# Kernel tuning notes

Hardware: AMD Instinct MI355X
Metric: run time of the kernel (lower is better)

Reference implementation:

```python
import jax, jax.numpy as jnp
import numpy as np

B, C_IN, C_OUT, A, H, W = 32, 256, 512, 256, 64, 64


def setup_inputs() -> dict:
    key = jax.random.key(0)
    ks = jax.random.split(key, 8)
    s = 0.02
    return {
        "x": jax.random.normal(ks[0], (B, C_IN, H, W), dtype=jnp.float32),
        "g": jax.random.normal(ks[1], (B, C_OUT), dtype=jnp.float32),
        "Wg": jax.random.normal(ks[2], (A, C_OUT), dtype=jnp.float32) * s,
        "bg": jnp.full((A,), 0.1, dtype=jnp.float32),
        "Wx": jax.random.normal(ks[3], (A, C_IN), dtype=jnp.float32) * s,
        "bx": jnp.full((A,), 0.1, dtype=jnp.float32),
        "Wf": jax.random.normal(ks[4], (1, A), dtype=jnp.float32) * s,
        "bf": jnp.full((1,), 0.1, dtype=jnp.float32),
    }


def reference(x, g, Wg, bg, Wx, bx, Wf, bf):
    b, c, h, w = x.shape
    gg = g @ Wg.T + bg                                  # [B, A]
    xf = x.reshape(b, c, h * w)                          # [B, C, HW]
    # Linear_x applied per spatial position (batched instead of python loop)
    nx = jnp.einsum('bcn,ac->bna', xf, Wx) + bx          # [B, HW, A]
    nx = jax.nn.relu(gg[:, None, :] + nx)                # [B, HW, A]
    att = jnp.einsum('bna,a->bn', nx, Wf[0]) + bf[0]     # [B, HW]
    # min-subtract, sum-divide normalization
    att = att - jnp.min(att, axis=1, keepdims=True)
    att = att / jnp.sum(att, axis=1, keepdims=True)
    out = jnp.einsum('bcn,bn->bc', xf, att)              # weighted pooling [B, C]
    return out, att.reshape(b, h, w)
```

## Files before the change

### kernel.cpp

```cpp
#include <hip/hip_runtime.h>
#include <stdint.h>

#define B_   32
#define CIN  256
#define COUT 512
#define A_   256
#define HW_  4096
#define NT   64

typedef short  short8  __attribute__((ext_vector_type(8)));
typedef float  float4_ __attribute__((ext_vector_type(4)));

__device__ __forceinline__ unsigned f2bf(float f) {
    unsigned u = __float_as_uint(f);
    u += 0x7FFFu + ((u >> 16) & 1u);
    return u >> 16;
}
__device__ __forceinline__ float bf2f(unsigned h) {
    return __uint_as_float(h << 16);
}

__global__ __launch_bounds__(256) void prep_kernel(
    const float* __restrict__ g, const float* __restrict__ Wg,
    const float* __restrict__ bg, const float* __restrict__ Wx,
    const float* __restrict__ bx,
    uint4* __restrict__ WxR, float* __restrict__ ggbx,
    float* __restrict__ P, float* __restrict__ T)
{
    int t = threadIdx.x;
    if (blockIdx.x >= 32) {
        int e = (blockIdx.x - 32) * 256 + t;
        int lane = e & 63, ai = (e >> 6) & 3, kk = (e >> 8) & 7, w = e >> 11;
        int a  = w * 64 + ai * 16 + (lane & 15);
        int kb = kk * 32 + (lane >> 4) * 8;
        const float4* s = (const float4*)(Wx + (size_t)a * 256 + kb);
        float4 u0 = s[0], u1 = s[1];
        uint4 pk;
        pk.x = f2bf(u0.x) | (f2bf(u0.y) << 16);
        pk.y = f2bf(u0.z) | (f2bf(u0.w) << 16);
        pk.z = f2bf(u1.x) | (f2bf(u1.y) << 16);
        pk.w = f2bf(u1.z) | (f2bf(u1.w) << 16);
        WxR[e] = pk;
        return;
    }
    int b = blockIdx.x;
    int i = b * 256 + t;
    P[i] = 0.f; T[i] = 0.f;

    __shared__ float gl[COUT];
    gl[t]       = g[b * COUT + t];
    gl[t + 256] = g[b * COUT + 256 + t];
    __syncthreads();

    float acc0 = bg[t] + bx[t], acc1 = 0.f;
    const float4* wr = (const float4*)(Wg + (size_t)t * COUT);
    #pragma unroll 8
    for (int co = 0; co < COUT / 4; co += 2) {
        float4 wv0 = wr[co],     gv0 = *(const float4*)&gl[co * 4];
        float4 wv1 = wr[co + 1], gv1 = *(const float4*)&gl[co * 4 + 4];
        acc0 += wv0.x * gv0.x + wv0.y * gv0.y + wv0.z * gv0.z + wv0.w * gv0.w;
        acc1 += wv1.x * gv1.x + wv1.y * gv1.y + wv1.z * gv1.z + wv1.w * gv1.w;
    }
    ggbx[b * 256 + t] = acc0 + acc1;
}

__global__ __launch_bounds__(256, 4) void attn_main(
    const float* __restrict__ x, const char* __restrict__ WxR,
    const float* __restrict__ ggbx, const float* __restrict__ Wf,
    const float* __restrict__ bfs,
    float* __restrict__ P, float* __restrict__ T, float* __restrict__ raw)
{
    __shared__ unsigned int xT[NT * 128];
    __shared__ float att_part[4][NT];
    __shared__ float raw_l[NT];

    int bid = blockIdx.x;
    int b = bid >> 6, nt = bid & 63;
    int t = threadIdx.x, w = t >> 6, lane = t & 63;
    int quad = lane >> 4, l15 = lane & 15;

    const float* xb = x + (size_t)b * CIN * HW_ + nt * NT;

    {
        int sub = lane >> 4;
        int n4  = (lane & 15) * 4;
        int cb0 = w * 64 + sub * 8;
        int cb1 = cb0 + 32;
        float4_ v[16];
        #pragma unroll
        for (int j = 0; j < 8; j++)
            v[j] = *(const float4_*)(xb + (size_t)(cb0 + j) * HW_ + n4);
        #pragma unroll
        for (int j = 0; j < 8; j++)
            v[8 + j] = *(const float4_*)(xb + (size_t)(cb1 + j) * HW_ + n4);

        #pragma unroll
        for (int gq = 0; gq < 2; gq++) {
            int q = (gq ? cb1 : cb0) >> 3;
            const float4_* vg = &v[gq * 8];
            #pragma unroll
            for (int r = 0; r < 4; r++) {
                uint4 pk;
                pk.x = f2bf(vg[0][r]) | (f2bf(vg[1][r]) << 16);
                pk.y = f2bf(vg[2][r]) | (f2bf(vg[3][r]) << 16);
                pk.z = f2bf(vg[4][r]) | (f2bf(vg[5][r]) << 16);
                pk.w = f2bf(vg[6][r]) | (f2bf(vg[7][r]) << 16);
                int n = n4 + r;
                *(uint4*)&xT[n * 128 + ((q ^ (n & 31)) << 2)] = pk;
            }
        }
    }

    float ga[4], wfv[4];
    #pragma unroll
    for (int ai = 0; ai < 4; ai++) {
        int a = w * 64 + ai * 16 + l15;
        ga[ai]  = ggbx[b * 256 + a];
        wfv[ai] = Wf[a];
    }
    __syncthreads();

    float4_ acc[4][4];
    #pragma unroll
    for (int mi = 0; mi < 4; mi++)
        #pragma unroll
        for (int ai = 0; ai < 4; ai++)
            acc[mi][ai] = (float4_){0.f, 0.f, 0.f, 0.f};

    const char* wsl = WxR + w * 32768 + lane * 16;
    short8 afA[4], bfA[4], afB[4], bfB[4];

    auto LD = [&](short8* af, short8* bf, int k0) {
        int qk = (k0 >> 3) + quad;
        #pragma unroll
        for (int mi = 0; mi < 4; mi++) {
            int n = mi * 16 + l15;
            af[mi] = *(const short8*)&xT[n * 128 + ((qk ^ (n & 31)) << 2)];
        }
        const char* wk = wsl + (k0 >> 5) * 4096;
        #pragma unroll
        for (int ai = 0; ai < 4; ai++)
            bf[ai] = *(const short8*)(wk + ai * 1024);
    };
    auto MM = [&](short8* af, short8* bf) {
        #pragma unroll
        for (int mi = 0; mi < 4; mi++)
            #pragma unroll
            for (int ai = 0; ai < 4; ai++)
                acc[mi][ai] = __builtin_amdgcn_mfma_f32_16x16x32_bf16(
                    af[mi], bf[ai], acc[mi][ai], 0, 0, 0);
    };

    LD(afA, bfA, 0);   LD(afB, bfB, 32);
    MM(afA, bfA);      LD(afA, bfA, 64);
    MM(afB, bfB);      LD(afB, bfB, 96);
    MM(afA, bfA);      LD(afA, bfA, 128);
    MM(afB, bfB);      LD(afB, bfB, 160);
    MM(afA, bfA);      LD(afA, bfA, 192);
    MM(afB, bfB);      LD(afB, bfB, 224);
    MM(afA, bfA);
    MM(afB, bfB);

    #pragma unroll
    for (int mi = 0; mi < 4; mi++) {
        float p[4] = {0.f, 0.f, 0.f, 0.f};
        #pragma unroll
        for (int ai = 0; ai < 4; ai++) {
            #pragma unroll
            for (int r = 0; r < 4; r++) {
                float vv = acc[mi][ai][r] + ga[ai];
                vv = fmaxf(vv, 0.f);
                p[r] = fmaf(vv, wfv[ai], p[r]);
            }
        }
        #pragma unroll
        for (int r = 0; r < 4; r++) {
            #pragma unroll
            for (int off = 1; off < 16; off <<= 1)
                p[r] += __shfl_xor(p[r], off, 16);
        }
        if (l15 == 0) {
            #pragma unroll
            for (int r = 0; r < 4; r++)
                att_part[w][mi * 16 + quad * 4 + r] = p[r];
        }
    }
    __syncthreads();

    if (t < NT) {
        float rv = att_part[0][t] + att_part[1][t] + att_part[2][t] + att_part[3][t] + bfs[0];
        raw[b * HW_ + nt * NT + t] = rv;
        raw_l[t] = rv;
    }
    __syncthreads();

    float pp[4] = {0.f, 0.f, 0.f, 0.f};
    float tt[4] = {0.f, 0.f, 0.f, 0.f};
    {
        int q    = (t & 63) >> 1;
        int half = (t & 1) * 8;
        int nb   = (t >> 6) * 16;
        #pragma unroll
        for (int i = 0; i < 16; i++) {
            int n = nb + i;
            uint2 u = *(const uint2*)((const char*)xT + n * 512 + ((q ^ (n & 31)) << 4) + half);
            float rv = raw_l[n];
            float x0 = bf2f(u.x & 0xFFFFu), x1 = bf2f(u.x >> 16);
            float x2 = bf2f(u.y & 0xFFFFu), x3 = bf2f(u.y >> 16);
            pp[0] = fmaf(x0, rv, pp[0]); tt[0] += x0;
            pp[1] = fmaf(x1, rv, pp[1]); tt[1] += x1;
            pp[2] = fmaf(x2, rv, pp[2]); tt[2] += x2;
            pp[3] = fmaf(x3, rv, pp[3]); tt[3] += x3;
        }
    }
    __syncthreads();
    {
        float* red = (float*)xT;
        float4_* pr = (float4_*)(red + w * 512);
        float4_* tr = (float4_*)(red + w * 512 + 256);
        pr[t & 63] = (float4_){pp[0], pp[1], pp[2], pp[3]};
        tr[t & 63] = (float4_){tt[0], tt[1], tt[2], tt[3]};
        __syncthreads();
        float Pc = red[t] + red[512 + t] + red[1024 + t] + red[1536 + t];
        float Tc = red[256 + t] + red[768 + t] + red[1280 + t] + red[1792 + t];
        atomicAdd(&P[b * 256 + t], Pc);
        atomicAdd(&T[b * 256 + t], Tc);
    }
}

__global__ __launch_bounds__(256) void finalize_kernel(
    const float* __restrict__ raw, const float* __restrict__ P,
    const float* __restrict__ T, float* __restrict__ out)
{
    int b = blockIdx.x, t = threadIdx.x;
    const float* r = raw + (size_t)b * HW_;
    float v[16];
    float mn = 3.4e38f, sm = 0.f;
    #pragma unroll
    for (int i = 0; i < 16; i++) {
        v[i] = r[t + 256 * i];
        mn = fminf(mn, v[i]);
        sm += v[i];
    }
    #pragma unroll
    for (int off = 1; off < 64; off <<= 1) {
        mn = fminf(mn, __shfl_xor(mn, off, 64));
        sm += __shfl_xor(sm, off, 64);
    }
    __shared__ float smn[4], ssm[4];
    int w = t >> 6;
    if ((t & 63) == 0) { smn[w] = mn; ssm[w] = sm; }
    __syncthreads();
    mn = fminf(fminf(smn[0], smn[1]), fminf(smn[2], smn[3]));
    sm = (ssm[0] + ssm[1]) + (ssm[2] + ssm[3]);
    float S = sm - 4096.f * mn;
    float inv = 1.f / S;

    float* att = out + B_ * CIN + (size_t)b * HW_;
    #pragma unroll
    for (int i = 0; i < 16; i++) att[t + 256 * i] = (v[i] - mn) * inv;

    int ic = b * 256 + t;
    out[ic] = (P[ic] - mn * T[ic]) * inv;
}

extern "C" void kernel_launch(void* const* d_in, const int* in_sizes, int n_in,
                              void* d_out, int out_size, void* d_ws, size_t ws_size,
                              hipStream_t stream)
{
    const float* x   = (const float*)d_in[0];
    const float* g   = (const float*)d_in[1];
    const float* Wg  = (const float*)d_in[2];
    const float* bg  = (const float*)d_in[3];
    const float* Wx  = (const float*)d_in[4];
    const float* bx  = (const float*)d_in[5];
    const float* Wf  = (const float*)d_in[6];
    const float* bf  = (const float*)d_in[7];
    float* out = (float*)d_out;

    char* wsb = (char*)d_ws;
    uint4* WxR  = (uint4*)wsb;
    float* ggbx = (float*)(wsb + 131072);
    float* P    = ggbx + 8192;
    float* T    = P + 8192;
    float* raw  = T + 8192;

    prep_kernel<<<64, 256, 0, stream>>>(g, Wg, bg, Wx, bx, WxR, ggbx, P, T);
    attn_main<<<2048, 256, 0, stream>>>(x, (const char*)WxR, ggbx, Wf, bf, P, T, raw);
    finalize_kernel<<<32, 256, 0, stream>>>(raw, P, T, out);
}
```

Baseline: 242.8 us.

## Stage x tile in LDS as fp32 via direct global-to-LDS loads

Replaces the register-staged fp32-to-bf16 transpose of the x tile with direct global_load_lds copies into a 64KB fp32 LDS tile. The bf16 conversion moves into the MFMA A-fragment loads, which now do scalar strided LDS reads and pack pairs per K step. The weighted-pooling epilogue reads the fp32 tile directly and uses shuffle reductions with per-channel atomics instead of a cross-wave LDS reduction. LDS use doubles, so occupancy is lowered to 2 blocks per CU. The conversion work and LDS reads in the MMA loop grow, and the atomic count rises.

```diff
diff --git a/kernel.cpp b/kernel.cpp
--- a/kernel.cpp
+++ b/kernel.cpp
@@ -4,7 +4,6 @@
 #define B_   32
 #define CIN  256
 #define COUT 512
-#define A_   256
 #define HW_  4096
 #define NT   64
 
@@ -15,9 +14,6 @@
     unsigned u = __float_as_uint(f);
     u += 0x7FFFu + ((u >> 16) & 1u);
     return u >> 16;
-}
-__device__ __forceinline__ float bf2f(unsigned h) {
-    return __uint_as_float(h << 16);
 }
 
 __global__ __launch_bounds__(256) void prep_kernel(
@@ -64,13 +60,13 @@
     ggbx[b * 256 + t] = acc0 + acc1;
 }
 
-__global__ __launch_bounds__(256, 4) void attn_main(
+__global__ __launch_bounds__(256, 2) void attn_main(
     const float* __restrict__ x, const char* __restrict__ WxR,
     const float* __restrict__ ggbx, const float* __restrict__ Wf,
     const float* __restrict__ bfs,
     float* __restrict__ P, float* __restrict__ T, float* __restrict__ raw)
 {
-    __shared__ unsigned int xT[NT * 128];
+    __shared__ float xTf[CIN * NT];
     __shared__ float att_part[4][NT];
     __shared__ float raw_l[NT];
 
@@ -82,32 +78,14 @@
     const float* xb = x + (size_t)b * CIN * HW_ + nt * NT;
 
     {
-        int sub = lane >> 4;
-        int n4  = (lane & 15) * 4;
-        int cb0 = w * 64 + sub * 8;
-        int cb1 = cb0 + 32;
-        float4_ v[16];
-        #pragma unroll
-        for (int j = 0; j < 8; j++)
-            v[j] = *(const float4_*)(xb + (size_t)(cb0 + j) * HW_ + n4);
-        #pragma unroll
-        for (int j = 0; j < 8; j++)
-            v[8 + j] = *(const float4_*)(xb + (size_t)(cb1 + j) * HW_ + n4);
-
-        #pragma unroll
-        for (int gq = 0; gq < 2; gq++) {
-            int q = (gq ? cb1 : cb0) >> 3;
-            const float4_* vg = &v[gq * 8];
-            #pragma unroll
-            for (int r = 0; r < 4; r++) {
-                uint4 pk;
-                pk.x = f2bf(vg[0][r]) | (f2bf(vg[1][r]) << 16);
-                pk.y = f2bf(vg[2][r]) | (f2bf(vg[3][r]) << 16);
-                pk.z = f2bf(vg[4][r]) | (f2bf(vg[5][r]) << 16);
-                pk.w = f2bf(vg[6][r]) | (f2bf(vg[7][r]) << 16);
-                int n = n4 + r;
-                *(uint4*)&xT[n * 128 + ((q ^ (n & 31)) << 2)] = pk;
-            }
+        const float* gl0 = xb + (size_t)(lane >> 4) * HW_ + (lane & 15) * 4;
+        #pragma unroll
+        for (int j = 0; j < 16; j++) {
+            int c0 = w * 64 + j * 4;
+            __builtin_amdgcn_global_load_lds(
+                (const __attribute__((address_space(1))) unsigned int*)(gl0 + (size_t)c0 * HW_),
+                (__attribute__((address_space(3))) unsigned int*)&xTf[c0 * 64],
+                16, 0, 0);
         }
     }
 
@@ -118,7 +96,6 @@
         ga[ai]  = ggbx[b * 256 + a];
         wfv[ai] = Wf[a];
     }
-    __syncthreads();
 
     float4_ acc[4][4];
     #pragma unroll
@@ -127,20 +104,31 @@
         for (int ai = 0; ai < 4; ai++)
             acc[mi][ai] = (float4_){0.f, 0.f, 0.f, 0.f};
 
+    __syncthreads();
+
     const char* wsl = WxR + w * 32768 + lane * 16;
     short8 afA[4], bfA[4], afB[4], bfB[4];
 
-    auto LD = [&](short8* af, short8* bf, int k0) {
-        int qk = (k0 >> 3) + quad;
-        #pragma unroll
-        for (int mi = 0; mi < 4; mi++) {
-            int n = mi * 16 + l15;
-            af[mi] = *(const short8*)&xT[n * 128 + ((qk ^ (n & 31)) << 2)];
-        }
+    auto LDB = [&](short8* bf, int k0) {
         const char* wk = wsl + (k0 >> 5) * 4096;
         #pragma unroll
         for (int ai = 0; ai < 4; ai++)
             bf[ai] = *(const short8*)(wk + ai * 1024);
+    };
+    auto LDA = [&](short8* af, int k0) {
+        int cb = k0 + quad * 8;
+        #pragma unroll
+        for (int mi = 0; mi < 4; mi++) {
+            const float* bse = &xTf[cb * 64 + mi * 16 + l15];
+            union { unsigned u[4]; short8 s; } cv;
+            #pragma unroll
+            for (int p = 0; p < 4; p++) {
+                float f0 = bse[(2 * p) * 64];
+                float f1 = bse[(2 * p + 1) * 64];
+                cv.u[p] = f2bf(f0) | (f2bf(f1) << 16);
+            }
+            af[mi] = cv.s;
+        }
     };
     auto MM = [&](short8* af, short8* bf) {
         #pragma unroll
@@ -151,13 +139,14 @@
                     af[mi], bf[ai], acc[mi][ai], 0, 0, 0);
     };
 
-    LD(afA, bfA, 0);   LD(afB, bfB, 32);
-    MM(afA, bfA);      LD(afA, bfA, 64);
-    MM(afB, bfB);      LD(afB, bfB, 96);
-    MM(afA, bfA);      LD(afA, bfA, 128);
-    MM(afB, bfB);      LD(afB, bfB, 160);
-    MM(afA, bfA);      LD(afA, bfA, 192);
-    MM(afB, bfB);      LD(afB, bfB, 224);
+    LDA(afA, 0);   LDB(bfA, 0);
+    LDA(afB, 32);  LDB(bfB, 32);
+    MM(afA, bfA);  LDA(afA, 64);  LDB(bfA, 64);
+    MM(afB, bfB);  LDA(afB, 96);  LDB(bfB, 96);
+    MM(afA, bfA);  LDA(afA, 128); LDB(bfA, 128);
+    MM(afB, bfB);  LDA(afB, 160); LDB(bfB, 160);
+    MM(afA, bfA);  LDA(afA, 192); LDB(bfA, 192);
+    MM(afB, bfB);  LDA(afB, 224); LDB(bfB, 224);
     MM(afA, bfA);
     MM(afB, bfB);
 
@@ -194,37 +183,24 @@
     }
     __syncthreads();
 
-    float pp[4] = {0.f, 0.f, 0.f, 0.f};
-    float tt[4] = {0.f, 0.f, 0.f, 0.f};
     {
-        int q    = (t & 63) >> 1;
-        int half = (t & 1) * 8;
-        int nb   = (t >> 6) * 16;
-        #pragma unroll
-        for (int i = 0; i < 16; i++) {
-            int n = nb + i;
-            uint2 u = *(const uint2*)((const char*)xT + n * 512 + ((q ^ (n & 31)) << 4) + half);
-            float rv = raw_l[n];
-            float x0 = bf2f(u.x & 0xFFFFu), x1 = bf2f(u.x >> 16);
-            float x2 = bf2f(u.y & 0xFFFFu), x3 = bf2f(u.y >> 16);
-            pp[0] = fmaf(x0, rv, pp[0]); tt[0] += x0;
-            pp[1] = fmaf(x1, rv, pp[1]); tt[1] += x1;
-            pp[2] = fmaf(x2, rv, pp[2]); tt[2] += x2;
-            pp[3] = fmaf(x3, rv, pp[3]); tt[3] += x3;
-        }
-    }
-    __syncthreads();
-    {
-        float* red = (float*)xT;
-        float4_* pr = (float4_*)(red + w * 512);
-        float4_* tr = (float4_*)(red + w * 512 + 256);
-        pr[t & 63] = (float4_){pp[0], pp[1], pp[2], pp[3]};
-        tr[t & 63] = (float4_){tt[0], tt[1], tt[2], tt[3]};
-        __syncthreads();
-        float Pc = red[t] + red[512 + t] + red[1024 + t] + red[1536 + t];
-        float Tc = red[256 + t] + red[768 + t] + red[1280 + t] + red[1792 + t];
-        atomicAdd(&P[b * 256 + t], Pc);
-        atomicAdd(&T[b * 256 + t], Tc);
+        float4_ rl = *(const float4_*)&raw_l[l15 * 4];
+        #pragma unroll
+        for (int ci = 0; ci < 16; ci++) {
+            int c = w * 64 + ci * 4 + quad;
+            float4_ xv = *(const float4_*)&xTf[c * 64 + l15 * 4];
+            float pp = xv[0] * rl[0] + xv[1] * rl[1] + xv[2] * rl[2] + xv[3] * rl[3];
+            float tt = (xv[0] + xv[1]) + (xv[2] + xv[3]);
+            #pragma unroll
+            for (int off = 1; off < 16; off <<= 1) {
+                pp += __shfl_xor(pp, off, 16);
+                tt += __shfl_xor(tt, off, 16);
+            }
+            if (l15 == 0) {
+                atomicAdd(&P[b * 256 + c], pp);
+                atomicAdd(&T[b * 256 + c], tt);
+            }
+        }
     }
 }
 
```

New measurement: 277.5 us. 1.14x slower.
